# Performance work log

Hardware: AMD Instinct MI355X
Metric: run time of the kernel (lower is better)

Reference implementation:

```python
import jax, jax.numpy as jnp
import numpy as np

NUM_CLASSES = 80
STRIDES = (8, 16, 32)


def _decode(p, stride):
    # p: [B, 5+C, H, W] raw head -> [B, HW, 5+C] decoded (xy in px, wh=exp*stride)
    B, C, H, W = p.shape
    ys, xs = jnp.meshgrid(jnp.arange(H), jnp.arange(W), indexing='ij')
    grid = jnp.stack([xs, ys], -1).reshape(H * W, 2).astype(p.dtype)
    out = p.reshape(B, C, H * W).transpose(0, 2, 1)
    xy = (out[..., :2] + grid) * stride
    wh = jnp.exp(out[..., 2:4]) * stride
    out = jnp.concatenate([xy, wh, out[..., 4:]], -1)
    es = jnp.full((H * W,), float(stride), p.dtype)
    return out, grid[:, 0], grid[:, 1], es


def _pairwise_iou(gt, pr):
    # gt [G,4] cxcywh, pr [A,4] -> [G,A]
    gt_tl = gt[:, None, :2] - gt[:, None, 2:] * 0.5
    gt_br = gt[:, None, :2] + gt[:, None, 2:] * 0.5
    pr_tl = pr[None, :, :2] - pr[None, :, 2:] * 0.5
    pr_br = pr[None, :, :2] + pr[None, :, 2:] * 0.5
    tl = jnp.maximum(gt_tl, pr_tl)
    br = jnp.minimum(gt_br, pr_br)
    en = jnp.all(tl < br, -1).astype(gt.dtype)
    inter = jnp.prod(br - tl, -1) * en
    a_gt = jnp.prod(gt[:, 2:], -1)[:, None]
    a_pr = jnp.prod(pr[:, 2:], -1)[None, :]
    return inter / (a_gt + a_pr - inter + 1e-16)


def _assign(gt_boxes, gt_cls, bbox, clsp, objp, xg, yg, es):
    # SimOTA assignment for one image (all fixed-shape; non-candidate anchors
    # are masked out via huge cost instead of boolean gather).
    G = gt_boxes.shape[0]
    xc = (xg + 0.5) * es  # [A] anchor centers
    yc = (yg + 0.5) * es
    gl = gt_boxes[:, 0:1] - 0.5 * gt_boxes[:, 2:3]
    gr = gt_boxes[:, 0:1] + 0.5 * gt_boxes[:, 2:3]
    gt_ = gt_boxes[:, 1:2] - 0.5 * gt_boxes[:, 3:4]
    gb = gt_boxes[:, 1:2] + 0.5 * gt_boxes[:, 3:4]
    in_box = (xc[None] > gl) & (xc[None] < gr) & (yc[None] > gt_) & (yc[None] < gb)  # [G,A]
    r = 2.5 * es[None]
    in_ctr = ((xc[None] > gt_boxes[:, 0:1] - r) & (xc[None] < gt_boxes[:, 0:1] + r)
              & (yc[None] > gt_boxes[:, 1:2] - r) & (yc[None] < gt_boxes[:, 1:2] + r))
    fg_cand = jnp.any(in_box, 0) | jnp.any(in_ctr, 0)  # [A]
    in_both = in_box & in_ctr  # [G,A]

    ious = _pairwise_iou(gt_boxes, bbox)  # [G,A]
    ious_m = jnp.where(fg_cand[None, :], ious, 0.0)
    iou_cost = -jnp.log(ious_m + 1e-8)

    # pairwise cls BCE cost: bce(sqrt(sigmoid(cls)*sigmoid(obj)), onehot(gt)).sum(-1)
    p = jnp.sqrt(jax.nn.sigmoid(clsp) * jax.nn.sigmoid(objp[:, None]))  # [A,C]
    lp = jnp.maximum(jnp.log(p), -100.0)
    l1p = jnp.maximum(jnp.log1p(-p), -100.0)
    t = jax.nn.one_hot(gt_cls, NUM_CLASSES, dtype=p.dtype)  # [G,C]
    cls_cost = -(jnp.einsum('ac,gc->ga', lp - l1p, t) + jnp.sum(l1p, -1)[None, :])

    cost = (cls_cost + 3.0 * iou_cost
            + 1e5 * (~in_both).astype(p.dtype)
            + 1e9 * (~fg_cand)[None, :].astype(p.dtype))

    # dynamic-k: k_g = clamp(sum(top10 ious), min=1)
    topk_ious, _ = jax.lax.top_k(ious_m, 10)
    dyn_k = jnp.clip(topk_ious.sum(-1).astype(jnp.int32), 1, None)  # [G]
    rank = jnp.argsort(jnp.argsort(cost, axis=1), axis=1)  # rank of each anchor per gt
    matching = (rank < dyn_k[:, None]) & fg_cand[None, :]  # [G,A]
    # resolve anchors matched to multiple gts: keep min-cost gt
    multi = matching.sum(0) > 1
    best = jnp.argmin(cost, 0)
    matching = jnp.where(multi[None, :], jnp.arange(G)[:, None] == best[None, :], matching)

    fg = jnp.any(matching, 0)  # [A]
    matched_gt = jnp.argmax(matching, 0)  # [A]
    pred_iou = jnp.sum(matching * ious, 0)  # [A]
    matched_cls = gt_cls[matched_gt]
    return fg, matched_gt, pred_iou, matched_cls


def _giou_loss(b, g):
    tl = jnp.maximum(b[..., :2] - b[..., 2:] * 0.5, g[..., :2] - g[..., 2:] * 0.5)
    br = jnp.minimum(b[..., :2] + b[..., 2:] * 0.5, g[..., :2] + g[..., 2:] * 0.5)
    area_b = jnp.prod(b[..., 2:], -1)
    area_g = jnp.prod(g[..., 2:], -1)
    en = jnp.all(tl < br, -1).astype(b.dtype)
    inter = jnp.prod(br - tl, -1) * en
    union = area_b + area_g - inter
    iou = inter / (union + 1e-16)
    ctl = jnp.minimum(b[..., :2] - b[..., 2:] * 0.5, g[..., :2] - g[..., 2:] * 0.5)
    cbr = jnp.maximum(b[..., :2] + b[..., 2:] * 0.5, g[..., :2] + g[..., 2:] * 0.5)
    area_c = jnp.maximum(jnp.prod(cbr - ctl, -1), 1e-16)
    giou = iou - (area_c - union) / area_c
    return 1.0 - jnp.clip(giou, -1.0, 1.0)


def _bce_logits(x, t):
    return jnp.maximum(x, 0.0) - x * t + jnp.log1p(jnp.exp(-jnp.abs(x)))


def _forward(p8, p16, p32, labels):
    outs, xo, yo, eo = [], [], [], []
    for p, s in zip((p8, p16, p32), STRIDES):
        o, x, y, e = _decode(p, s)
        outs.append(o); xo.append(x); yo.append(y); eo.append(e)
    outputs = jnp.concatenate(outs, 1)  # [B, A, 5+C]
    xg = jnp.concatenate(xo); yg = jnp.concatenate(yo); es = jnp.concatenate(eo)

    bbox = outputs[..., :4]
    obj = outputs[..., 4]
    cls = outputs[..., 5:]
    gt_boxes = labels[..., :4]
    gt_cls = labels[..., 4].astype(jnp.int32)

    # assignment runs under no_grad in torch
    det = jax.lax.stop_gradient(outputs)
    fg, matched_gt, pred_iou, matched_cls = jax.vmap(
        lambda gb, gc, o: _assign(gb, gc, o[..., :4], o[..., 5:], o[..., 4], xg, yg, es)
    )(gt_boxes, gt_cls, det)

    fgf = fg.astype(outputs.dtype)  # [B,A]
    reg_t = jnp.take_along_axis(gt_boxes, matched_gt[..., None], axis=1)  # [B,A,4]
    cls_t = (jax.nn.one_hot(matched_cls, NUM_CLASSES, dtype=outputs.dtype)
             * pred_iou[..., None] * fgf[..., None])

    loss_iou = jnp.sum(_giou_loss(bbox, reg_t) * fgf)
    loss_obj = jnp.sum(_bce_logits(obj, fgf))
    loss_cls = jnp.sum(_bce_logits(cls, cls_t) * fgf[..., None])
    num_fg = jnp.maximum(jnp.sum(fgf), 1.0)
    return (5.0 * loss_iou + loss_obj + loss_cls) / num_fg


def setup_inputs() -> dict:
    key = jax.random.key(0)
    k1, k2, k3, k4, k5, k6 = jax.random.split(key, 6)
    B, NGT = 32, 20
    p8 = jax.random.normal(k1, (B, 5 + NUM_CLASSES, 80, 80), dtype=jnp.float32)
    p16 = jax.random.normal(k2, (B, 5 + NUM_CLASSES, 40, 40), dtype=jnp.float32)
    p32 = jax.random.normal(k3, (B, 5 + NUM_CLASSES, 20, 20), dtype=jnp.float32)
    cxy = jax.random.uniform(k4, (B, NGT, 2), dtype=jnp.float32, minval=32.0, maxval=608.0)
    wh = jax.random.uniform(k5, (B, NGT, 2), dtype=jnp.float32, minval=16.0, maxval=128.0)
    cls = jax.random.randint(k6, (B, NGT, 1), 0, NUM_CLASSES).astype(jnp.float32)
    labels = jnp.concatenate([cxy, wh, cls], -1)
    return {"p8": p8, "p16": p16, "p32": p32, "labels": labels}


def reference(p8, p16, p32, labels):
    return _forward(p8, p16, p32, labels)
```

## Files before the change

kernel.cpp:

```cpp
#include <hip/hip_runtime.h>
#include <cstdint>
#include <cstddef>

#define NA 8400
#define NAP 8448
#define NB 32
#define NG 20
#define NCL 80

__device__ __forceinline__ float frcp(float x) { return __builtin_amdgcn_rcpf(x); }
__device__ __forceinline__ float bce0(float x) {
  return fmaxf(x, 0.0f) + __logf(1.0f + __expf(-fabsf(x)));
}

__device__ __forceinline__ void anchor_info(int a, const float* p8, const float* p16,
                                            const float* p32, int b, const float*& base,
                                            int& hw, int& HW, int& xg, int& yg, float& fs) {
  if (a < 6400)      { hw = a;        HW = 6400; xg = hw % 80; yg = hw / 80; fs = 8.f;
                       base = p8  + (size_t)b * 85 * 6400; }
  else if (a < 8000) { hw = a - 6400; HW = 1600; xg = hw % 40; yg = hw / 40; fs = 16.f;
                       base = p16 + (size_t)b * 85 * 1600; }
  else               { hw = a - 8000; HW = 400;  xg = hw % 20; yg = hw / 20; fs = 32.f;
                       base = p32 + (size_t)b * 85 * 400; }
}

__device__ __forceinline__ float iou_raw(float gx, float gy, float gw, float gh, float4 p) {
  float gtlx = gx - gw * 0.5f, gtly = gy - gh * 0.5f;
  float gbrx = gx + gw * 0.5f, gbry = gy + gh * 0.5f;
  float ptlx = p.x - p.z * 0.5f, ptly = p.y - p.w * 0.5f;
  float pbrx = p.x + p.z * 0.5f, pbry = p.y + p.w * 0.5f;
  float tlx = fmaxf(gtlx, ptlx), tly = fmaxf(gtly, ptly);
  float brx = fminf(gbrx, pbrx), bry = fminf(gbry, pbry);
  float inter = ((tlx < brx) && (tly < bry)) ? (brx - tlx) * (bry - tly) : 0.0f;
  float ag = gw * gh, ap = p.z * p.w;
  return inter * frcp(ag + ap - inter + 1e-16f);
}

__device__ __forceinline__ float giou_loss(float4 bb, float gx, float gy, float gw, float gh) {
  float btlx = bb.x - bb.z * 0.5f, btly = bb.y - bb.w * 0.5f;
  float bbrx = bb.x + bb.z * 0.5f, bbry = bb.y + bb.w * 0.5f;
  float gtlx = gx - gw * 0.5f, gtly = gy - gh * 0.5f;
  float gbrx = gx + gw * 0.5f, gbry = gy + gh * 0.5f;
  float tlx = fmaxf(btlx, gtlx), tly = fmaxf(btly, gtly);
  float brx = fminf(bbrx, gbrx), bry = fminf(bbry, gbry);
  float area_b = bb.z * bb.w, area_g = gw * gh;
  float inter = ((tlx < brx) && (tly < bry)) ? (brx - tlx) * (bry - tly) : 0.0f;
  float uni = area_b + area_g - inter;
  float iou = inter / (uni + 1e-16f);
  float ctlx = fminf(btlx, gtlx), ctly = fminf(btly, gtly);
  float cbrx = fmaxf(bbrx, gbrx), cbry = fmaxf(bbry, gbry);
  float area_c = fmaxf((cbrx - ctlx) * (cbry - ctly), 1e-16f);
  float giou = iou - (area_c - uni) / area_c;
  giou = fminf(fmaxf(giou, -1.0f), 1.0f);
  return 1.0f - giou;
}

__device__ __forceinline__ void block_argmin(float& v, int& i, volatile float* s_v,
                                             volatile int* s_i, int tid) {
#pragma unroll
  for (int off = 32; off; off >>= 1) {
    float ov = __shfl_down(v, off, 64);
    int   oi = __shfl_down(i, off, 64);
    if (ov < v || (ov == v && oi < i)) { v = ov; i = oi; }
  }
  if ((tid & 63) == 0) { s_v[tid >> 6] = v; s_i[tid >> 6] = i; }
  __syncthreads();
  v = s_v[0]; i = s_i[0];
#pragma unroll
  for (int w = 1; w < 4; ++w) {
    float ov = s_v[w]; int oi = s_i[w];
    if (ov < v || (ov == v && oi < i)) { v = ov; i = oi; }
  }
}

__global__ __launch_bounds__(1024) void kA0(const float* __restrict__ p8,
                                            const float* __restrict__ p16,
                                            const float* __restrict__ p32,
                                            const float* __restrict__ labels,
                                            unsigned int* __restrict__ am_c,
                                            int* __restrict__ fg_list,
                                            int* __restrict__ n_fg,
                                            unsigned int* __restrict__ match_c,
                                            float* __restrict__ accum) {
  __shared__ float s_gt[NG * 4];
  __shared__ unsigned int s_wcnt[16];
  __shared__ unsigned int s_base;
  __shared__ float s_part[16];
  int b = blockIdx.x, tid = threadIdx.x, lane = tid & 63, wid = tid >> 6;
  if (tid < NG) {
    s_gt[tid * 4 + 0] = labels[((size_t)b * NG + tid) * 5 + 0];
    s_gt[tid * 4 + 1] = labels[((size_t)b * NG + tid) * 5 + 1];
    s_gt[tid * 4 + 2] = labels[((size_t)b * NG + tid) * 5 + 2];
    s_gt[tid * 4 + 3] = labels[((size_t)b * NG + tid) * 5 + 3];
  }
  if (tid == 0) s_base = 0u;
  __syncthreads();

  float bce_obj = 0.0f;
  for (int it = 0; it < 9; ++it) {
    int a = it * 1024 + tid;
    unsigned int msk = 0u;
    bool fg = false;
    if (a < NA) {
      const float* base; int hw, HW, xg, yg; float fs;
      anchor_info(a, p8, p16, p32, b, base, hw, HW, xg, yg, fs);
      float obj = base[4 * HW + hw];
      bce_obj += bce0(obj);
      float xc = ((float)xg + 0.5f) * fs;
      float yc = ((float)yg + 0.5f) * fs;
      float r = 2.5f * fs;
#pragma unroll
      for (int g = 0; g < NG; ++g) {
        float gx = s_gt[g * 4 + 0], gy = s_gt[g * 4 + 1];
        float gw = s_gt[g * 4 + 2], gh = s_gt[g * 4 + 3];
        bool inb = (xc > gx - 0.5f * gw) && (xc < gx + 0.5f * gw) &&
                   (yc > gy - 0.5f * gh) && (yc < gy + 0.5f * gh);
        bool inc = (xc > gx - r) && (xc < gx + r) && (yc > gy - r) && (yc < gy + r);
        fg = fg || inb || inc;
        if (inb && inc) msk |= (1u << g);
      }
    }
    if (a < NAP) match_c[(size_t)b * NAP + a] = 0u;

    unsigned long long bm = __ballot(fg);
    if (lane == 0) s_wcnt[wid] = (unsigned int)__popcll(bm);
    __syncthreads();
    unsigned int pos = s_base;
    for (int w = 0; w < wid; ++w) pos += s_wcnt[w];
    if (fg) {
      pos += (unsigned int)__popcll(bm & ((1ull << lane) - 1ull));
      fg_list[(size_t)b * NAP + pos] = a;
      am_c[(size_t)b * NAP + pos] = msk | 0x80000000u;
    }
    __syncthreads();
    if (tid == 0) {
      unsigned int t = 0;
      for (int w = 0; w < 16; ++w) t += s_wcnt[w];
      s_base += t;
    }
    __syncthreads();
  }
  if (tid == 0) n_fg[b] = (int)s_base;

#pragma unroll
  for (int off = 32; off; off >>= 1) bce_obj += __shfl_down(bce_obj, off, 64);
  if (lane == 0) s_part[wid] = bce_obj;
  __syncthreads();
  if (tid == 0) {
    float t = 0.0f;
    for (int w = 0; w < 16; ++w) t += s_part[w];
    atomicAdd(&accum[1], t);
  }
}

__global__ __launch_bounds__(256) void kA1(const float* __restrict__ p8,
                                           const float* __restrict__ p16,
                                           const float* __restrict__ p32,
                                           const float* __restrict__ labels,
                                           const int* __restrict__ fg_list,
                                           const int* __restrict__ n_fg,
                                           float4* __restrict__ bbox_c,
                                           float* __restrict__ sl_c,
                                           float* __restrict__ sb_c,
                                           float* __restrict__ w_c) {
  __shared__ unsigned int s_gmask[NCL];
  int b = blockIdx.y, tid = threadIdx.x;
  if (tid < NCL) s_gmask[tid] = 0u;
  __syncthreads();
  if (tid < NG) {
    int c = (int)labels[((size_t)b * NG + tid) * 5 + 4];
    atomicOr(&s_gmask[c], 1u << tid);
  }
  __syncthreads();

  int n = n_fg[b];
  for (int ci = blockIdx.x * 256 + tid; ci < n; ci += gridDim.x * 256) {
    int a = fg_list[(size_t)b * NAP + ci];
    const float* base; int hw, HW, xg, yg; float fs;
    anchor_info(a, p8, p16, p32, b, base, hw, HW, xg, yg, fs);

    float obj = base[4 * HW + hw];
    float v0 = base[hw];
    float v1 = base[HW + hw];
    float v2 = base[2 * HW + hw];
    float v3 = base[3 * HW + hw];
    bbox_c[(size_t)b * NAP + ci] = make_float4((v0 + (float)xg) * fs, (v1 + (float)yg) * fs,
                                               __expf(v2) * fs, __expf(v3) * fs);
    float uo  = __logf(1.0f + __expf(-fabsf(obj)));
    float lso = fminf(obj, 0.0f) - uo;

    float sl = 0.0f, sb = 0.0f;
    for (int cc = 0; cc < NCL; cc += 8) {
      float xs[8];
#pragma unroll
      for (int j = 0; j < 8; ++j) xs[j] = base[(5 + cc + j) * HW + hw];
#pragma unroll
      for (int j = 0; j < 8; ++j) {
        float x = xs[j];
        float u = __logf(1.0f + __expf(-fabsf(x)));
        sb += fmaxf(x, 0.0f) + u;
        float lsx = fminf(x, 0.0f) - u;
        float lpr = 0.5f * (lsx + lso);
        float p   = __expf(lpr);
        float l1p = fmaxf(__logf(1.0f - p), -100.0f);
        sl += l1p;
        unsigned int m = s_gmask[cc + j];
        if (m) {
          float w = fmaxf(lpr, -100.0f) - l1p;
          do {
            int g = __ffs(m) - 1; m &= m - 1;
            w_c[((size_t)b * NG + g) * NAP + ci] = w;
          } while (m);
        }
      }
    }
    sl_c[(size_t)b * NAP + ci] = sl;
    sb_c[(size_t)b * NAP + ci] = sb;
  }
}

__global__ __launch_bounds__(256) void kB(const float* __restrict__ labels,
                                          const float4* __restrict__ bbox_c,
                                          const float* __restrict__ sl_c,
                                          const float* __restrict__ w_c,
                                          const unsigned int* __restrict__ am_c,
                                          const int* __restrict__ n_fg,
                                          unsigned int* __restrict__ match_c) {
  __shared__ float s_cost[NAP];
  __shared__ float s_wt[4 * 10];
  __shared__ float s_v[4];
  __shared__ int   s_i[4];
  __shared__ int   s_k;

  int g = blockIdx.x, b = blockIdx.y, tid = threadIdx.x;
  int lane = tid & 63, wid = tid >> 6;
  int n = n_fg[b];
  size_t bo = (size_t)b * NAP;
  const float* __restrict__ wg = w_c + ((size_t)b * NG + g) * NAP;

  float gx = labels[((size_t)b * NG + g) * 5 + 0];
  float gy = labels[((size_t)b * NG + g) * 5 + 1];
  float gw = labels[((size_t)b * NG + g) * 5 + 2];
  float gh = labels[((size_t)b * NG + g) * 5 + 3];

  float t10[10];
#pragma unroll
  for (int j = 0; j < 10; ++j) t10[j] = 0.0f;

  for (int ci = tid; ci < n; ci += 256) {
    unsigned int am = am_c[bo + ci];
    float wv = wg[ci];
    float sl = sl_c[bo + ci];
    float4 pb = bbox_c[bo + ci];
    float iou = iou_raw(gx, gy, gw, gh, pb);
    if (iou > t10[9]) {
      t10[9] = iou;
#pragma unroll
      for (int q = 9; q > 0; --q) {
        if (t10[q] > t10[q - 1]) { float t = t10[q]; t10[q] = t10[q - 1]; t10[q - 1] = t; }
        else break;
      }
    }
    float c = -(wv + sl) - 3.0f * __logf(iou + 1e-8f);
    if (!((am >> g) & 1u)) c += 100000.0f;
    s_cost[ci] = c;
  }

  for (int r = 0; r < 10; ++r) {
    float v = t10[0];
    float bv = v;
#pragma unroll
    for (int off = 32; off; off >>= 1) bv = fmaxf(bv, __shfl_down(bv, off, 64));
    bv = __shfl(bv, 0, 64);
    unsigned long long won = __ballot(v == bv);
    if (lane == __ffsll(won) - 1) {
#pragma unroll
      for (int q = 0; q < 9; ++q) t10[q] = t10[q + 1];
      t10[9] = -1.0f;
    }
    if (lane == 0) s_wt[wid * 10 + r] = bv;
  }
  __syncthreads();

  if (tid == 0) {
    int p0 = 0, p1 = 0, p2 = 0, p3 = 0;
    float s = 0.0f;
    for (int r = 0; r < 10; ++r) {
      float v0 = (p0 < 10) ? s_wt[p0]      : -2.0f;
      float v1 = (p1 < 10) ? s_wt[10 + p1] : -2.0f;
      float v2 = (p2 < 10) ? s_wt[20 + p2] : -2.0f;
      float v3 = (p3 < 10) ? s_wt[30 + p3] : -2.0f;
      float m = fmaxf(fmaxf(v0, v1), fmaxf(v2, v3));
      s += m;
      if (m == v0) ++p0; else if (m == v1) ++p1; else if (m == v2) ++p2; else ++p3;
    }
    int k = (int)s;
    if (k < 1) k = 1;
    s_k = k;
  }
  __syncthreads();
  int k = s_k;

  for (int it = 0; it < k; ++it) {
    float bv = 3.4e38f; int bi = NAP;
    for (int ci = tid; ci < n; ci += 256) {
      float v = s_cost[ci];
      if (v < bv || (v == bv && ci < bi)) { bv = v; bi = ci; }
    }
    block_argmin(bv, bi, s_v, s_i, tid);
    if (bv >= 1e8f) break;
    if (tid == 0) {
      atomicOr(&match_c[bo + bi], 1u << g);
      s_cost[bi] = 3.4e38f;
    }
    __syncthreads();
  }
}

__global__ __launch_bounds__(256) void kC(const float* __restrict__ p8,
                                          const float* __restrict__ p16,
                                          const float* __restrict__ p32,
                                          const float* __restrict__ labels,
                                          const float4* __restrict__ bbox_c,
                                          const float* __restrict__ sl_c,
                                          const float* __restrict__ sb_c,
                                          const float* __restrict__ w_c,
                                          const unsigned int* __restrict__ am_c,
                                          const int* __restrict__ fg_list,
                                          const int* __restrict__ n_fg,
                                          const unsigned int* __restrict__ match_c,
                                          float* __restrict__ accum) {
  __shared__ float s_gt[NG * 5];
  __shared__ float s_red[16];
  int b = blockIdx.y, tid = threadIdx.x;
  if (tid < NG * 5) s_gt[tid] = labels[(size_t)b * NG * 5 + tid];
  __syncthreads();

  int n = n_fg[b];
  size_t bo = (size_t)b * NAP;
  float li = 0.0f, oe = 0.0f, lc = 0.0f, nf = 0.0f;

  for (int ci = blockIdx.x * 256 + tid; ci < n; ci += gridDim.x * 256) {
    unsigned int m = match_c[bo + ci];
    if (m == 0u) continue;
    int a = fg_list[bo + ci];
    const float* base; int hw, HW, xg, yg; float fs;
    anchor_info(a, p8, p16, p32, b, base, hw, HW, xg, yg, fs);
    float4 pb = bbox_c[bo + ci];
    int mg;
    if (m & (m - 1)) {
      unsigned int am = am_c[bo + ci];
      float sl = sl_c[bo + ci];
      float bestc = 3.4e38f; mg = 0;
#pragma unroll 4
      for (int g = 0; g < NG; ++g) {
        float iou = iou_raw(s_gt[g * 5], s_gt[g * 5 + 1], s_gt[g * 5 + 2], s_gt[g * 5 + 3], pb);
        float wv = w_c[((size_t)b * NG + g) * NAP + ci];
        float c = -(wv + sl) - 3.0f * __logf(iou + 1e-8f);
        if (!((am >> g) & 1u)) c += 100000.0f;
        if (c < bestc) { bestc = c; mg = g; }
      }
    } else {
      mg = __ffs(m) - 1;
    }
    float gx = s_gt[mg * 5], gy = s_gt[mg * 5 + 1];
    float gw = s_gt[mg * 5 + 2], gh = s_gt[mg * 5 + 3];
    int cg = (int)s_gt[mg * 5 + 4];
    float piou = iou_raw(gx, gy, gw, gh, pb);
    li += giou_loss(pb, gx, gy, gw, gh);
    float xcls = base[(5 + cg) * HW + hw];
    lc += sb_c[bo + ci] - xcls * piou;
    oe += base[4 * HW + hw];
    nf += 1.0f;
  }

  float vals[4] = {li, oe, lc, nf};
#pragma unroll
  for (int q = 0; q < 4; ++q) {
#pragma unroll
    for (int off = 32; off; off >>= 1) vals[q] += __shfl_down(vals[q], off, 64);
  }
  if ((tid & 63) == 0) {
    int wid = tid >> 6;
    s_red[wid * 4 + 0] = vals[0];
    s_red[wid * 4 + 1] = vals[1];
    s_red[wid * 4 + 2] = vals[2];
    s_red[wid * 4 + 3] = vals[3];
  }
  __syncthreads();
  if (tid < 4) {
    const int slot[4] = {0, 2, 3, 4};
    float s = s_red[tid] + s_red[4 + tid] + s_red[8 + tid] + s_red[12 + tid];
    atomicAdd(&accum[slot[tid]], s);
  }
}

__global__ void kD(const float* __restrict__ accum, float* __restrict__ out) {
  float loss_iou = accum[0];
  float loss_obj = accum[1] - accum[2];
  float loss_cls = accum[3];
  float num_fg = fmaxf(accum[4], 1.0f);
  out[0] = (5.0f * loss_iou + loss_obj + loss_cls) / num_fg;
}

extern "C" void kernel_launch(void* const* d_in, const int* in_sizes, int n_in,
                              void* d_out, int out_size, void* d_ws, size_t ws_size,
                              hipStream_t stream) {
  const float* p8     = (const float*)d_in[0];
  const float* p16    = (const float*)d_in[1];
  const float* p32    = (const float*)d_in[2];
  const float* labels = (const float*)d_in[3];
  float* out = (float*)d_out;

  const size_t BAP = (size_t)NB * NAP;
  char* w = (char*)d_ws;
  float4*       bbox_c  = (float4*)w;
  float*        w_c     = (float*)(w + BAP * 16);
  char*         w2      = w + BAP * 16 + (size_t)NB * NG * NAP * 4;
  int*          fg_list = (int*)(w2);
  unsigned int* am_c    = (unsigned int*)(w2 + BAP * 4);
  unsigned int* match_c = (unsigned int*)(w2 + BAP * 8);
  float*        sl_c    = (float*)(w2 + BAP * 12);
  float*        sb_c    = (float*)(w2 + BAP * 16);
  int*          n_fg    = (int*)(w2 + BAP * 20);
  float*        accum   = (float*)(w2 + BAP * 20 + 128);

  hipMemsetAsync(accum, 0, 32, stream);

  kA0<<<dim3(NB), dim3(1024), 0, stream>>>(p8, p16, p32, labels, am_c, fg_list, n_fg,
                                           match_c, accum);
  kA1<<<dim3(12, NB), dim3(256), 0, stream>>>(p8, p16, p32, labels, fg_list, n_fg,
                                              bbox_c, sl_c, sb_c, w_c);
  kB<<<dim3(NG, NB), dim3(256), 0, stream>>>(labels, bbox_c, sl_c, w_c, am_c, n_fg, match_c);
  kC<<<dim3(12, NB), dim3(256), 0, stream>>>(p8, p16, p32, labels, bbox_c, sl_c, sb_c, w_c,
                                             am_c, fg_list, n_fg, match_c, accum);
  kD<<<1, 1, 0, stream>>>(accum, out);
}
```

Before: 196.5 us.

## Split serial per-image compaction into count and scan-scatter kernels across many blocks

```diff
diff --git a/kernel.cpp b/kernel.cpp
--- a/kernel.cpp
+++ b/kernel.cpp
@@ -7,6 +7,7 @@
 #define NB 32
 #define NG 20
 #define NCL 80
+#define NBLK 33
 
 __device__ __forceinline__ float frcp(float x) { return __builtin_amdgcn_rcpf(x); }
 __device__ __forceinline__ float bce0(float x) {
@@ -22,6 +23,15 @@
                        base = p16 + (size_t)b * 85 * 1600; }
   else               { hw = a - 8000; HW = 400;  xg = hw % 20; yg = hw / 20; fs = 32.f;
                        base = p32 + (size_t)b * 85 * 400; }
+}
+
+__device__ __forceinline__ void anchor_xy(int a, float& xc, float& yc, float& fs) {
+  int xg, yg;
+  if (a < 6400)      { xg = a % 80; yg = a / 80; fs = 8.f; }
+  else if (a < 8000) { int h = a - 6400; xg = h % 40; yg = h / 40; fs = 16.f; }
+  else               { int h = a - 8000; xg = h % 20; yg = h / 20; fs = 32.f; }
+  xc = ((float)xg + 0.5f) * fs;
+  yc = ((float)yg + 0.5f) * fs;
 }
 
 __device__ __forceinline__ float iou_raw(float gx, float gy, float gw, float gh, float4 p) {
@@ -73,83 +83,106 @@
   }
 }
 
-__global__ __launch_bounds__(1024) void kA0(const float* __restrict__ p8,
-                                            const float* __restrict__ p16,
-                                            const float* __restrict__ p32,
-                                            const float* __restrict__ labels,
-                                            unsigned int* __restrict__ am_c,
-                                            int* __restrict__ fg_list,
-                                            int* __restrict__ n_fg,
-                                            unsigned int* __restrict__ match_c,
-                                            float* __restrict__ accum) {
+__device__ __forceinline__ void geom_mask(int a, const float* s_gt, bool& fg,
+                                          unsigned int& msk) {
+  float xc, yc, fs;
+  anchor_xy(a, xc, yc, fs);
+  float r = 2.5f * fs;
+  fg = false; msk = 0u;
+#pragma unroll
+  for (int g = 0; g < NG; ++g) {
+    float gx = s_gt[g * 4 + 0], gy = s_gt[g * 4 + 1];
+    float gw = s_gt[g * 4 + 2], gh = s_gt[g * 4 + 3];
+    bool inb = (xc > gx - 0.5f * gw) && (xc < gx + 0.5f * gw) &&
+               (yc > gy - 0.5f * gh) && (yc < gy + 0.5f * gh);
+    bool inc = (xc > gx - r) && (xc < gx + r) && (yc > gy - r) && (yc < gy + r);
+    fg = fg || inb || inc;
+    if (inb && inc) msk |= (1u << g);
+  }
+}
+
+__global__ __launch_bounds__(256) void kG(const float* __restrict__ p8,
+                                          const float* __restrict__ p16,
+                                          const float* __restrict__ p32,
+                                          const float* __restrict__ labels,
+                                          unsigned int* __restrict__ blk_cnt,
+                                          unsigned int* __restrict__ match_c,
+                                          float* __restrict__ accum) {
   __shared__ float s_gt[NG * 4];
-  __shared__ unsigned int s_wcnt[16];
-  __shared__ unsigned int s_base;
-  __shared__ float s_part[16];
-  int b = blockIdx.x, tid = threadIdx.x, lane = tid & 63, wid = tid >> 6;
+  __shared__ unsigned int s_wcnt[4];
+  __shared__ float s_part[4];
+  int blk = blockIdx.x, b = blockIdx.y, tid = threadIdx.x, lane = tid & 63, wid = tid >> 6;
   if (tid < NG) {
     s_gt[tid * 4 + 0] = labels[((size_t)b * NG + tid) * 5 + 0];
     s_gt[tid * 4 + 1] = labels[((size_t)b * NG + tid) * 5 + 1];
     s_gt[tid * 4 + 2] = labels[((size_t)b * NG + tid) * 5 + 2];
     s_gt[tid * 4 + 3] = labels[((size_t)b * NG + tid) * 5 + 3];
   }
-  if (tid == 0) s_base = 0u;
-  __syncthreads();
-
+  __syncthreads();
+
+  int a = blk * 256 + tid;
+  match_c[(size_t)b * NAP + a] = 0u;
+  bool fg = false;
+  unsigned int msk;
   float bce_obj = 0.0f;
-  for (int it = 0; it < 9; ++it) {
-    int a = it * 1024 + tid;
-    unsigned int msk = 0u;
-    bool fg = false;
-    if (a < NA) {
-      const float* base; int hw, HW, xg, yg; float fs;
-      anchor_info(a, p8, p16, p32, b, base, hw, HW, xg, yg, fs);
-      float obj = base[4 * HW + hw];
-      bce_obj += bce0(obj);
-      float xc = ((float)xg + 0.5f) * fs;
-      float yc = ((float)yg + 0.5f) * fs;
-      float r = 2.5f * fs;
-#pragma unroll
-      for (int g = 0; g < NG; ++g) {
-        float gx = s_gt[g * 4 + 0], gy = s_gt[g * 4 + 1];
-        float gw = s_gt[g * 4 + 2], gh = s_gt[g * 4 + 3];
-        bool inb = (xc > gx - 0.5f * gw) && (xc < gx + 0.5f * gw) &&
-                   (yc > gy - 0.5f * gh) && (yc < gy + 0.5f * gh);
-        bool inc = (xc > gx - r) && (xc < gx + r) && (yc > gy - r) && (yc < gy + r);
-        fg = fg || inb || inc;
-        if (inb && inc) msk |= (1u << g);
-      }
-    }
-    if (a < NAP) match_c[(size_t)b * NAP + a] = 0u;
-
-    unsigned long long bm = __ballot(fg);
-    if (lane == 0) s_wcnt[wid] = (unsigned int)__popcll(bm);
-    __syncthreads();
+  if (a < NA) {
+    const float* base; int hw, HW, xg, yg; float fs;
+    anchor_info(a, p8, p16, p32, b, base, hw, HW, xg, yg, fs);
+    bce_obj = bce0(base[4 * HW + hw]);
+    geom_mask(a, s_gt, fg, msk);
+  }
+  unsigned long long bm = __ballot(fg);
+#pragma unroll
+  for (int off = 32; off; off >>= 1) bce_obj += __shfl_down(bce_obj, off, 64);
+  if (lane == 0) { s_wcnt[wid] = (unsigned int)__popcll(bm); s_part[wid] = bce_obj; }
+  __syncthreads();
+  if (tid == 0) {
+    blk_cnt[b * NBLK + blk] = s_wcnt[0] + s_wcnt[1] + s_wcnt[2] + s_wcnt[3];
+    atomicAdd(&accum[1], s_part[0] + s_part[1] + s_part[2] + s_part[3]);
+  }
+}
+
+__global__ __launch_bounds__(256) void kX(const float* __restrict__ labels,
+                                          const unsigned int* __restrict__ blk_cnt,
+                                          int* __restrict__ fg_list,
+                                          unsigned int* __restrict__ am_c,
+                                          int* __restrict__ n_fg) {
+  __shared__ float s_gt[NG * 4];
+  __shared__ unsigned int s_wcnt[4];
+  __shared__ unsigned int s_base;
+  int blk = blockIdx.x, b = blockIdx.y, tid = threadIdx.x, lane = tid & 63, wid = tid >> 6;
+  if (tid < NG) {
+    s_gt[tid * 4 + 0] = labels[((size_t)b * NG + tid) * 5 + 0];
+    s_gt[tid * 4 + 1] = labels[((size_t)b * NG + tid) * 5 + 1];
+    s_gt[tid * 4 + 2] = labels[((size_t)b * NG + tid) * 5 + 2];
+    s_gt[tid * 4 + 3] = labels[((size_t)b * NG + tid) * 5 + 3];
+  }
+  if (wid == 0) {
+    unsigned int c = (lane < NBLK) ? blk_cnt[b * NBLK + lane] : 0u;
+    unsigned int p = c;
+#pragma unroll
+    for (int off = 1; off < 64; off <<= 1) {
+      unsigned int t = __shfl_up(p, off, 64);
+      if (lane >= off) p += t;
+    }
+    if (lane == (unsigned)blk) s_base = p - c;
+    if (blk == 0 && lane == NBLK - 1) n_fg[b] = (int)p;
+  }
+  __syncthreads();
+
+  int a = blk * 256 + tid;
+  bool fg = false;
+  unsigned int msk = 0u;
+  if (a < NA) geom_mask(a, s_gt, fg, msk);
+  unsigned long long bm = __ballot(fg);
+  if (lane == 0) s_wcnt[wid] = (unsigned int)__popcll(bm);
+  __syncthreads();
+  if (fg) {
     unsigned int pos = s_base;
     for (int w = 0; w < wid; ++w) pos += s_wcnt[w];
-    if (fg) {
-      pos += (unsigned int)__popcll(bm & ((1ull << lane) - 1ull));
-      fg_list[(size_t)b * NAP + pos] = a;
-      am_c[(size_t)b * NAP + pos] = msk | 0x80000000u;
-    }
-    __syncthreads();
-    if (tid == 0) {
-      unsigned int t = 0;
-      for (int w = 0; w < 16; ++w) t += s_wcnt[w];
-      s_base += t;
-    }
-    __syncthreads();
-  }
-  if (tid == 0) n_fg[b] = (int)s_base;
-
-#pragma unroll
-  for (int off = 32; off; off >>= 1) bce_obj += __shfl_down(bce_obj, off, 64);
-  if (lane == 0) s_part[wid] = bce_obj;
-  __syncthreads();
-  if (tid == 0) {
-    float t = 0.0f;
-    for (int w = 0; w < 16; ++w) t += s_part[w];
-    atomicAdd(&accum[1], t);
+    pos += (unsigned int)__popcll(bm & ((1ull << lane) - 1ull));
+    fg_list[(size_t)b * NAP + pos] = a;
+    am_c[(size_t)b * NAP + pos] = msk | 0x80000000u;
   }
 }
 
@@ -424,11 +457,12 @@
   float*        sb_c    = (float*)(w2 + BAP * 16);
   int*          n_fg    = (int*)(w2 + BAP * 20);
   float*        accum   = (float*)(w2 + BAP * 20 + 128);
+  unsigned int* blk_cnt = (unsigned int*)(w2 + BAP * 20 + 256);
 
   hipMemsetAsync(accum, 0, 32, stream);
 
-  kA0<<<dim3(NB), dim3(1024), 0, stream>>>(p8, p16, p32, labels, am_c, fg_list, n_fg,
-                                           match_c, accum);
+  kG<<<dim3(NBLK, NB), dim3(256), 0, stream>>>(p8, p16, p32, labels, blk_cnt, match_c, accum);
+  kX<<<dim3(NBLK, NB), dim3(256), 0, stream>>>(labels, blk_cnt, fg_list, am_c, n_fg);
   kA1<<<dim3(12, NB), dim3(256), 0, stream>>>(p8, p16, p32, labels, fg_list, n_fg,
                                               bbox_c, sl_c, sb_c, w_c);
   kB<<<dim3(NG, NB), dim3(256), 0, stream>>>(labels, bbox_c, sl_c, w_c, am_c, n_fg, match_c);
```

New measurement: 182.7 us. 1.08x faster.

## Fuse candidate selection with feature gather and fold final combine into last block

Applied to the files above, without the earlier changes.

```diff
diff --git a/kernel.cpp b/kernel.cpp
--- a/kernel.cpp
+++ b/kernel.cpp
@@ -7,6 +7,8 @@
 #define NB 32
 #define NG 20
 #define NCL 80
+#define NBLK 33
+#define KC_BLKS 12
 
 __device__ __forceinline__ float frcp(float x) { return __builtin_amdgcn_rcpf(x); }
 __device__ __forceinline__ float bce0(float x) {
@@ -73,99 +75,33 @@
   }
 }
 
-__global__ __launch_bounds__(1024) void kA0(const float* __restrict__ p8,
+__global__ __launch_bounds__(256) void kGXA(const float* __restrict__ p8,
                                             const float* __restrict__ p16,
                                             const float* __restrict__ p32,
                                             const float* __restrict__ labels,
+                                            int* __restrict__ n_fg_cnt,
+                                            int* __restrict__ fg_list,
                                             unsigned int* __restrict__ am_c,
-                                            int* __restrict__ fg_list,
-                                            int* __restrict__ n_fg,
+                                            float4* __restrict__ bbox_c,
+                                            float* __restrict__ sl_c,
+                                            float* __restrict__ sb_c,
+                                            float* __restrict__ w_c,
                                             unsigned int* __restrict__ match_c,
-                                            float* __restrict__ accum) {
+                                            float* __restrict__ blk_obj) {
   __shared__ float s_gt[NG * 4];
-  __shared__ unsigned int s_wcnt[16];
+  __shared__ unsigned int s_gmask[NCL];
+  __shared__ unsigned int s_wcnt[4];
+  __shared__ float s_part[4];
   __shared__ unsigned int s_base;
-  __shared__ float s_part[16];
-  int b = blockIdx.x, tid = threadIdx.x, lane = tid & 63, wid = tid >> 6;
+  int blk = blockIdx.x, b = blockIdx.y, tid = threadIdx.x, lane = tid & 63, wid = tid >> 6;
+
+  if (tid < NCL) s_gmask[tid] = 0u;
   if (tid < NG) {
     s_gt[tid * 4 + 0] = labels[((size_t)b * NG + tid) * 5 + 0];
     s_gt[tid * 4 + 1] = labels[((size_t)b * NG + tid) * 5 + 1];
     s_gt[tid * 4 + 2] = labels[((size_t)b * NG + tid) * 5 + 2];
     s_gt[tid * 4 + 3] = labels[((size_t)b * NG + tid) * 5 + 3];
   }
-  if (tid == 0) s_base = 0u;
-  __syncthreads();
-
-  float bce_obj = 0.0f;
-  for (int it = 0; it < 9; ++it) {
-    int a = it * 1024 + tid;
-    unsigned int msk = 0u;
-    bool fg = false;
-    if (a < NA) {
-      const float* base; int hw, HW, xg, yg; float fs;
-      anchor_info(a, p8, p16, p32, b, base, hw, HW, xg, yg, fs);
-      float obj = base[4 * HW + hw];
-      bce_obj += bce0(obj);
-      float xc = ((float)xg + 0.5f) * fs;
-      float yc = ((float)yg + 0.5f) * fs;
-      float r = 2.5f * fs;
-#pragma unroll
-      for (int g = 0; g < NG; ++g) {
-        float gx = s_gt[g * 4 + 0], gy = s_gt[g * 4 + 1];
-        float gw = s_gt[g * 4 + 2], gh = s_gt[g * 4 + 3];
-        bool inb = (xc > gx - 0.5f * gw) && (xc < gx + 0.5f * gw) &&
-                   (yc > gy - 0.5f * gh) && (yc < gy + 0.5f * gh);
-        bool inc = (xc > gx - r) && (xc < gx + r) && (yc > gy - r) && (yc < gy + r);
-        fg = fg || inb || inc;
-        if (inb && inc) msk |= (1u << g);
-      }
-    }
-    if (a < NAP) match_c[(size_t)b * NAP + a] = 0u;
-
-    unsigned long long bm = __ballot(fg);
-    if (lane == 0) s_wcnt[wid] = (unsigned int)__popcll(bm);
-    __syncthreads();
-    unsigned int pos = s_base;
-    for (int w = 0; w < wid; ++w) pos += s_wcnt[w];
-    if (fg) {
-      pos += (unsigned int)__popcll(bm & ((1ull << lane) - 1ull));
-      fg_list[(size_t)b * NAP + pos] = a;
-      am_c[(size_t)b * NAP + pos] = msk | 0x80000000u;
-    }
-    __syncthreads();
-    if (tid == 0) {
-      unsigned int t = 0;
-      for (int w = 0; w < 16; ++w) t += s_wcnt[w];
-      s_base += t;
-    }
-    __syncthreads();
-  }
-  if (tid == 0) n_fg[b] = (int)s_base;
-
-#pragma unroll
-  for (int off = 32; off; off >>= 1) bce_obj += __shfl_down(bce_obj, off, 64);
-  if (lane == 0) s_part[wid] = bce_obj;
-  __syncthreads();
-  if (tid == 0) {
-    float t = 0.0f;
-    for (int w = 0; w < 16; ++w) t += s_part[w];
-    atomicAdd(&accum[1], t);
-  }
-}
-
-__global__ __launch_bounds__(256) void kA1(const float* __restrict__ p8,
-                                           const float* __restrict__ p16,
-                                           const float* __restrict__ p32,
-                                           const float* __restrict__ labels,
-                                           const int* __restrict__ fg_list,
-                                           const int* __restrict__ n_fg,
-                                           float4* __restrict__ bbox_c,
-                                           float* __restrict__ sl_c,
-                                           float* __restrict__ sb_c,
-                                           float* __restrict__ w_c) {
-  __shared__ unsigned int s_gmask[NCL];
-  int b = blockIdx.y, tid = threadIdx.x;
-  if (tid < NCL) s_gmask[tid] = 0u;
   __syncthreads();
   if (tid < NG) {
     int c = (int)labels[((size_t)b * NG + tid) * 5 + 4];
@@ -173,50 +109,89 @@
   }
   __syncthreads();
 
-  int n = n_fg[b];
-  for (int ci = blockIdx.x * 256 + tid; ci < n; ci += gridDim.x * 256) {
-    int a = fg_list[(size_t)b * NAP + ci];
-    const float* base; int hw, HW, xg, yg; float fs;
+  int a = blk * 256 + tid;
+  match_c[(size_t)b * NAP + a] = 0u;
+
+  bool fg = false;
+  unsigned int msk = 0u;
+  float bce_obj = 0.0f, obj = 0.0f;
+  const float* base = nullptr; int hw = 0, HW = 0, xg = 0, yg = 0; float fs = 8.f;
+  if (a < NA) {
     anchor_info(a, p8, p16, p32, b, base, hw, HW, xg, yg, fs);
-
-    float obj = base[4 * HW + hw];
-    float v0 = base[hw];
-    float v1 = base[HW + hw];
-    float v2 = base[2 * HW + hw];
-    float v3 = base[3 * HW + hw];
-    bbox_c[(size_t)b * NAP + ci] = make_float4((v0 + (float)xg) * fs, (v1 + (float)yg) * fs,
-                                               __expf(v2) * fs, __expf(v3) * fs);
-    float uo  = __logf(1.0f + __expf(-fabsf(obj)));
-    float lso = fminf(obj, 0.0f) - uo;
-
-    float sl = 0.0f, sb = 0.0f;
-    for (int cc = 0; cc < NCL; cc += 8) {
-      float xs[8];
-#pragma unroll
-      for (int j = 0; j < 8; ++j) xs[j] = base[(5 + cc + j) * HW + hw];
-#pragma unroll
-      for (int j = 0; j < 8; ++j) {
-        float x = xs[j];
-        float u = __logf(1.0f + __expf(-fabsf(x)));
-        sb += fmaxf(x, 0.0f) + u;
-        float lsx = fminf(x, 0.0f) - u;
-        float lpr = 0.5f * (lsx + lso);
-        float p   = __expf(lpr);
-        float l1p = fmaxf(__logf(1.0f - p), -100.0f);
-        sl += l1p;
-        unsigned int m = s_gmask[cc + j];
-        if (m) {
-          float w = fmaxf(lpr, -100.0f) - l1p;
-          do {
-            int g = __ffs(m) - 1; m &= m - 1;
-            w_c[((size_t)b * NG + g) * NAP + ci] = w;
-          } while (m);
-        }
+    obj = base[4 * HW + hw];
+    bce_obj = bce0(obj);
+    float xc = ((float)xg + 0.5f) * fs;
+    float yc = ((float)yg + 0.5f) * fs;
+    float r = 2.5f * fs;
+#pragma unroll
+    for (int g = 0; g < NG; ++g) {
+      float gx = s_gt[g * 4 + 0], gy = s_gt[g * 4 + 1];
+      float gw = s_gt[g * 4 + 2], gh = s_gt[g * 4 + 3];
+      bool inb = (xc > gx - 0.5f * gw) && (xc < gx + 0.5f * gw) &&
+                 (yc > gy - 0.5f * gh) && (yc < gy + 0.5f * gh);
+      bool inc = (xc > gx - r) && (xc < gx + r) && (yc > gy - r) && (yc < gy + r);
+      fg = fg || inb || inc;
+      if (inb && inc) msk |= (1u << g);
+    }
+  }
+
+  unsigned long long bm = __ballot(fg);
+#pragma unroll
+  for (int off = 32; off; off >>= 1) bce_obj += __shfl_down(bce_obj, off, 64);
+  if (lane == 0) { s_wcnt[wid] = (unsigned int)__popcll(bm); s_part[wid] = bce_obj; }
+  __syncthreads();
+  if (tid == 0) {
+    unsigned int cnt = s_wcnt[0] + s_wcnt[1] + s_wcnt[2] + s_wcnt[3];
+    s_base = cnt ? (unsigned int)atomicAdd(&n_fg_cnt[b], (int)cnt) : 0u;
+    blk_obj[b * NBLK + blk] = s_part[0] + s_part[1] + s_part[2] + s_part[3];
+  }
+  __syncthreads();
+
+  if (!fg) return;
+  unsigned int pos = s_base;
+  for (int w = 0; w < wid; ++w) pos += s_wcnt[w];
+  pos += (unsigned int)__popcll(bm & ((1ull << lane) - 1ull));
+  int ci = (int)pos;
+  size_t bo = (size_t)b * NAP;
+  fg_list[bo + ci] = a;
+  am_c[bo + ci] = msk | 0x80000000u;
+
+  float v0 = base[hw];
+  float v1 = base[HW + hw];
+  float v2 = base[2 * HW + hw];
+  float v3 = base[3 * HW + hw];
+  bbox_c[bo + ci] = make_float4((v0 + (float)xg) * fs, (v1 + (float)yg) * fs,
+                                __expf(v2) * fs, __expf(v3) * fs);
+  float uo  = __logf(1.0f + __expf(-fabsf(obj)));
+  float lso = fminf(obj, 0.0f) - uo;
+
+  float sl = 0.0f, sb = 0.0f;
+  for (int cc = 0; cc < NCL; cc += 8) {
+    float xs[8];
+#pragma unroll
+    for (int j = 0; j < 8; ++j) xs[j] = base[(5 + cc + j) * HW + hw];
+#pragma unroll
+    for (int j = 0; j < 8; ++j) {
+      float x = xs[j];
+      float u = __logf(1.0f + __expf(-fabsf(x)));
+      sb += fmaxf(x, 0.0f) + u;
+      float lsx = fminf(x, 0.0f) - u;
+      float lpr = 0.5f * (lsx + lso);
+      float p   = __expf(lpr);
+      float l1p = fmaxf(__logf(1.0f - p), -100.0f);
+      sl += l1p;
+      unsigned int m = s_gmask[cc + j];
+      if (m) {
+        float w = fmaxf(lpr, -100.0f) - l1p;
+        do {
+          int g = __ffs(m) - 1; m &= m - 1;
+          w_c[((size_t)b * NG + g) * NAP + ci] = w;
+        } while (m);
       }
     }
-    sl_c[(size_t)b * NAP + ci] = sl;
-    sb_c[(size_t)b * NAP + ci] = sb;
-  }
+  }
+  sl_c[bo + ci] = sl;
+  sb_c[bo + ci] = sb;
 }
 
 __global__ __launch_bounds__(256) void kB(const float* __restrict__ labels,
@@ -317,21 +292,25 @@
   }
 }
 
-__global__ __launch_bounds__(256) void kC(const float* __restrict__ p8,
-                                          const float* __restrict__ p16,
-                                          const float* __restrict__ p32,
-                                          const float* __restrict__ labels,
-                                          const float4* __restrict__ bbox_c,
-                                          const float* __restrict__ sl_c,
-                                          const float* __restrict__ sb_c,
-                                          const float* __restrict__ w_c,
-                                          const unsigned int* __restrict__ am_c,
-                                          const int* __restrict__ fg_list,
-                                          const int* __restrict__ n_fg,
-                                          const unsigned int* __restrict__ match_c,
-                                          float* __restrict__ accum) {
+__global__ __launch_bounds__(256) void kCD(const float* __restrict__ p8,
+                                           const float* __restrict__ p16,
+                                           const float* __restrict__ p32,
+                                           const float* __restrict__ labels,
+                                           const float4* __restrict__ bbox_c,
+                                           const float* __restrict__ sl_c,
+                                           const float* __restrict__ sb_c,
+                                           const float* __restrict__ w_c,
+                                           const unsigned int* __restrict__ am_c,
+                                           const int* __restrict__ fg_list,
+                                           const int* __restrict__ n_fg,
+                                           const unsigned int* __restrict__ match_c,
+                                           const float* __restrict__ blk_obj,
+                                           float* __restrict__ accum,
+                                           int* __restrict__ done_cnt,
+                                           float* __restrict__ out) {
   __shared__ float s_gt[NG * 5];
   __shared__ float s_red[16];
+  __shared__ int s_last;
   int b = blockIdx.y, tid = threadIdx.x;
   if (tid < NG * 5) s_gt[tid] = labels[(size_t)b * NG * 5 + tid];
   __syncthreads();
@@ -340,7 +319,7 @@
   size_t bo = (size_t)b * NAP;
   float li = 0.0f, oe = 0.0f, lc = 0.0f, nf = 0.0f;
 
-  for (int ci = blockIdx.x * 256 + tid; ci < n; ci += gridDim.x * 256) {
+  for (int ci = blockIdx.x * 256 + tid; ci < n; ci += KC_BLKS * 256) {
     unsigned int m = match_c[bo + ci];
     if (m == 0u) continue;
     int a = fg_list[bo + ci];
@@ -393,14 +372,30 @@
     float s = s_red[tid] + s_red[4 + tid] + s_red[8 + tid] + s_red[12 + tid];
     atomicAdd(&accum[slot[tid]], s);
   }
-}
-
-__global__ void kD(const float* __restrict__ accum, float* __restrict__ out) {
-  float loss_iou = accum[0];
-  float loss_obj = accum[1] - accum[2];
-  float loss_cls = accum[3];
-  float num_fg = fmaxf(accum[4], 1.0f);
-  out[0] = (5.0f * loss_iou + loss_obj + loss_cls) / num_fg;
+
+  if (tid == 0) {
+    __threadfence();
+    int old = atomicAdd(done_cnt, 1);
+    s_last = (old == KC_BLKS * NB - 1) ? 1 : 0;
+  }
+  __syncthreads();
+  if (s_last) {
+    float s = 0.0f;
+    for (int i = tid; i < NB * NBLK; i += 256) s += blk_obj[i];
+#pragma unroll
+    for (int off = 32; off; off >>= 1) s += __shfl_down(s, off, 64);
+    if ((tid & 63) == 0) s_red[tid >> 6] = s;
+    __syncthreads();
+    if (tid == 0) {
+      float obj_base = s_red[0] + s_red[1] + s_red[2] + s_red[3];
+      float loss_iou = atomicAdd(&accum[0], 0.0f);
+      float oex      = atomicAdd(&accum[2], 0.0f);
+      float loss_cls = atomicAdd(&accum[3], 0.0f);
+      float num_fg   = atomicAdd(&accum[4], 0.0f);
+      float loss_obj = obj_base - oex;
+      out[0] = (5.0f * loss_iou + loss_obj + loss_cls) / fmaxf(num_fg, 1.0f);
+    }
+  }
 }
 
 extern "C" void kernel_launch(void* const* d_in, const int* in_sizes, int n_in,
@@ -422,17 +417,18 @@
   unsigned int* match_c = (unsigned int*)(w2 + BAP * 8);
   float*        sl_c    = (float*)(w2 + BAP * 12);
   float*        sb_c    = (float*)(w2 + BAP * 16);
-  int*          n_fg    = (int*)(w2 + BAP * 20);
-  float*        accum   = (float*)(w2 + BAP * 20 + 128);
-
-  hipMemsetAsync(accum, 0, 32, stream);
-
-  kA0<<<dim3(NB), dim3(1024), 0, stream>>>(p8, p16, p32, labels, am_c, fg_list, n_fg,
-                                           match_c, accum);
-  kA1<<<dim3(12, NB), dim3(256), 0, stream>>>(p8, p16, p32, labels, fg_list, n_fg,
-                                              bbox_c, sl_c, sb_c, w_c);
+  char*         w3      = w2 + BAP * 20;
+  int*          n_fg    = (int*)w3;
+  float*        accum   = (float*)(w3 + 128);
+  int*          done_cnt= (int*)(w3 + 160);
+  float*        blk_obj = (float*)(w3 + 256);
+
+  hipMemsetAsync(w3, 0, 256, stream);
+
+  kGXA<<<dim3(NBLK, NB), dim3(256), 0, stream>>>(p8, p16, p32, labels, n_fg, fg_list, am_c,
+                                                 bbox_c, sl_c, sb_c, w_c, match_c, blk_obj);
   kB<<<dim3(NG, NB), dim3(256), 0, stream>>>(labels, bbox_c, sl_c, w_c, am_c, n_fg, match_c);
-  kC<<<dim3(12, NB), dim3(256), 0, stream>>>(p8, p16, p32, labels, bbox_c, sl_c, sb_c, w_c,
-                                             am_c, fg_list, n_fg, match_c, accum);
-  kD<<<1, 1, 0, stream>>>(accum, out);
-}
+  kCD<<<dim3(KC_BLKS, NB), dim3(256), 0, stream>>>(p8, p16, p32, labels, bbox_c, sl_c, sb_c,
+                                                   w_c, am_c, fg_list, n_fg, match_c, blk_obj,
+                                                   accum, done_cnt, out);
+}
```

Result: faster. 181.7 us (-7.6%).
